# Kernel optimization log

Measured on AMD Instinct MI355X. Metric: run time of the kernel, lower is better.

The kernel has to match this reference:

```python
import jax, jax.numpy as jnp
import numpy as np

BLOCK_SIZE = 32
# E2M1 (FP4) representable magnitudes and rounding midpoints
FP4_GRID = jnp.array([0.0, 0.5, 1.0, 1.5, 2.0, 3.0, 4.0, 6.0], dtype=jnp.float32)
FP4_MIDS = jnp.array([0.25, 0.75, 1.25, 1.75, 2.5, 3.5, 5.0], dtype=jnp.float32)


def quantize_to_mxfp4(w, block_size=BLOCK_SIZE):
    """Quantize (K, N) weight to MXFP4: per-block-of-32 (along K) power-of-2 scale
    + E2M1 codes. Returns dequantized-code tensor q (K//bs, bs, N) and scales
    (K//bs, 1, N) so that dequant = q * scales."""
    K, N = w.shape
    wb = w.reshape(K // block_size, block_size, N)
    amax = jnp.max(jnp.abs(wb), axis=1, keepdims=True)          # (K//bs, 1, N)
    # E8M0 scale: 2^(floor(log2(amax)) - 2) so amax/scale falls in [4, 8) -> clipped to 6
    exp = jnp.floor(jnp.log2(jnp.maximum(amax, 1e-30))) - 2.0
    scales = jnp.exp2(exp)
    x = wb / scales
    idx = jnp.digitize(jnp.abs(x), FP4_MIDS)                    # round-to-nearest FP4 magnitude
    q = jnp.sign(x) * FP4_GRID[idx]
    return q, scales


def mxfp4_matmul(inputs, q, scales, block_size=BLOCK_SIZE):
    """inputs: (..., K); q: (K//bs, bs, N); scales: (K//bs, 1, N)."""
    K = inputs.shape[-1]
    N = q.shape[-1]
    w = (q * scales).reshape(K, N)   # fused dequant (reference form)
    return inputs @ w


def setup_inputs() -> dict:
    key = jax.random.key(0)
    ks = jax.random.split(key, 3)
    B, S, D, F = 4, 2048, 2048, 8192
    inputs = jax.random.normal(ks[0], (B, S, D), dtype=jnp.float32)
    up_kernel = jax.random.normal(ks[1], (D, F), dtype=jnp.float32) * (1.0 / np.sqrt(D))
    down_kernel = jax.random.normal(ks[2], (F, D), dtype=jnp.float32) * (1.0 / np.sqrt(F))
    up_bias = jnp.zeros((F,), dtype=jnp.float32)
    down_bias = jnp.zeros((D,), dtype=jnp.float32)
    return {"inputs": inputs, "up_kernel": up_kernel, "up_bias": up_bias,
            "down_kernel": down_kernel, "down_bias": down_bias}


def reference(inputs, up_kernel, up_bias, down_kernel, down_bias):
    q_up, s_up = quantize_to_mxfp4(up_kernel, BLOCK_SIZE)
    x = mxfp4_matmul(inputs, q_up, s_up, BLOCK_SIZE) + up_bias
    x = jax.nn.gelu(x)
    q_dn, s_dn = quantize_to_mxfp4(down_kernel, BLOCK_SIZE)
    x = mxfp4_matmul(x, q_dn, s_dn, BLOCK_SIZE) + down_bias
    return x
```

## Files before the change

### kernel.cpp

```cpp
#include <hip/hip_runtime.h>
#include <hip/hip_bf16.h>

typedef __bf16 bf16_t;
typedef __attribute__((ext_vector_type(8))) __bf16 bf16x8;
typedef __attribute__((ext_vector_type(4))) float f32x4;
typedef __attribute__((ext_vector_type(4))) unsigned int u32x4;

__device__ __forceinline__ void gload_lds16(const bf16_t* g, bf16_t* l) {
    __builtin_amdgcn_global_load_lds(
        (const __attribute__((address_space(1))) void*)g,
        (__attribute__((address_space(3))) void*)l,
        16, 0, 0);
}

__device__ __forceinline__ float gelu_f(float v) {
    float u = 0.7978845608028654f * (v + 0.044715f * v * v * v);
    float e = __expf(-2.f * u);
    float t = __fdividef(1.f - e, 1.f + e);
    return 0.5f * v * (1.f + t);
}

__global__ void cvt_kernel(const float* __restrict__ in, bf16_t* __restrict__ out, int n) {
    int i = (blockIdx.x * blockDim.x + threadIdx.x) << 3;
    if (i >= n) return;
    const f32x4* p = (const f32x4*)(in + i);
    f32x4 a = __builtin_nontemporal_load(p);
    f32x4 b = __builtin_nontemporal_load(p + 1);
    bf16x8 o;
    o[0] = (bf16_t)a[0]; o[1] = (bf16_t)a[1]; o[2] = (bf16_t)a[2]; o[3] = (bf16_t)a[3];
    o[4] = (bf16_t)b[0]; o[5] = (bf16_t)b[1]; o[6] = (bf16_t)b[2]; o[7] = (bf16_t)b[3];
    *(bf16x8*)(out + i) = o;
}

__global__ void quantize_kernel(const float* __restrict__ w, bf16_t* __restrict__ wt,
                                int K, int N) {
    int tid = blockIdx.x * blockDim.x + threadIdx.x;
    int total = (K >> 5) * N;
    if (tid >= total) return;
    int n = tid % N;
    int b = tid / N;
    const float* src = w + (size_t)b * 32 * N + n;
    float v[32];
    float amax = 0.f;
#pragma unroll
    for (int i = 0; i < 32; ++i) {
        v[i] = __builtin_nontemporal_load(src + (size_t)i * N);
        amax = fmaxf(amax, fabsf(v[i]));
    }
    unsigned eb = (__float_as_uint(amax) >> 23) & 0xFF;
    float scale = __uint_as_float((eb - 2u) << 23);
    float inv   = __uint_as_float((256u - eb) << 23);
    if (amax == 0.f) { scale = 0.f; inv = 0.f; }
    bf16_t dq[32];
#pragma unroll
    for (int i = 0; i < 32; ++i) {
        float x  = v[i] * inv;
        float ax = fabsf(x);
        float q = ax < 0.25f ? 0.0f : ax < 0.75f ? 0.5f : ax < 1.25f ? 1.0f :
                  ax < 1.75f ? 1.5f : ax < 2.5f  ? 2.0f : ax < 3.5f  ? 3.0f :
                  ax < 5.0f  ? 4.0f : 6.0f;
        float d = copysignf(q * scale, x);
        dq[i] = (bf16_t)d;
    }
    bf16_t* dst = wt + (size_t)n * K + b * 32;
#pragma unroll
    for (int j = 0; j < 4; ++j) {
        bf16x8 p;
#pragma unroll
        for (int t = 0; t < 8; ++t) p[t] = dq[j * 8 + t];
        *(bf16x8*)(dst + j * 8) = p;
    }
}

#define VMW4  asm volatile("s_waitcnt vmcnt(4)" ::: "memory")
#define VMW0  asm volatile("s_waitcnt vmcnt(0)" ::: "memory")
#define BARR  asm volatile("s_barrier" ::: "memory")
#define LGKM0 asm volatile("s_waitcnt lgkmcnt(0)" ::: "memory")

#define MFMA_ROW(MI, A0, A1)                                                          \
    acc[MI][0] = __builtin_amdgcn_mfma_f32_16x16x32_bf16(A0, bf00, acc[MI][0],0,0,0); \
    acc[MI][0] = __builtin_amdgcn_mfma_f32_16x16x32_bf16(A1, bf01, acc[MI][0],0,0,0); \
    acc[MI][1] = __builtin_amdgcn_mfma_f32_16x16x32_bf16(A0, bf10, acc[MI][1],0,0,0); \
    acc[MI][1] = __builtin_amdgcn_mfma_f32_16x16x32_bf16(A1, bf11, acc[MI][1],0,0,0); \
    acc[MI][2] = __builtin_amdgcn_mfma_f32_16x16x32_bf16(A0, bf20, acc[MI][2],0,0,0); \
    acc[MI][2] = __builtin_amdgcn_mfma_f32_16x16x32_bf16(A1, bf21, acc[MI][2],0,0,0); \
    acc[MI][3] = __builtin_amdgcn_mfma_f32_16x16x32_bf16(A0, bf30, acc[MI][3],0,0,0); \
    acc[MI][3] = __builtin_amdgcn_mfma_f32_16x16x32_bf16(A1, bf31, acc[MI][3],0,0,0);

#define PHASE(BUF, P, STAGE_STMT, TAIL_STMT)                                          \
  {                                                                                   \
    af00 = lda(BUF, 2*(P),   0); af01 = lda(BUF, 2*(P),   1);                         \
    af10 = lda(BUF, 2*(P)+1, 0); af11 = lda(BUF, 2*(P)+1, 1);                         \
    if ((P) == 0) {                                                                   \
      bf00 = ldb(BUF,0,0); bf01 = ldb(BUF,0,1);                                       \
      bf10 = ldb(BUF,1,0); bf11 = ldb(BUF,1,1);                                       \
      bf20 = ldb(BUF,2,0); bf21 = ldb(BUF,2,1);                                       \
      bf30 = ldb(BUF,3,0); bf31 = ldb(BUF,3,1);                                       \
    }                                                                                 \
    STAGE_STMT;                                                                       \
    BARR;                                                                             \
    LGKM0;                                                                            \
    __builtin_amdgcn_s_setprio(1);                                                    \
    MFMA_ROW(2*(P),   af00, af01);                                                    \
    MFMA_ROW(2*(P)+1, af10, af11);                                                    \
    __builtin_amdgcn_s_setprio(0);                                                    \
    TAIL_STMT;                                                                        \
    BARR;                                                                             \
  }

template <int EPI, int MAP>
__global__ __launch_bounds__(512, 2)
void gemm_kernel(const bf16_t* __restrict__ A, const bf16_t* __restrict__ Bt,
                 const float* __restrict__ bias, void* __restrict__ Cout,
                 int M, int N, int K) {
    __shared__ __align__(16) char smem[131072];
    bf16_t* sAp = (bf16_t*)smem;
    bf16_t* sBp = (bf16_t*)(smem + 65536);
    const int tid     = threadIdx.x;
    const int lane    = tid & 63;
    const int wv      = tid >> 6;
    const int wr      = wv >> 2;
    const int wc      = wv & 3;
    const int laneLow = lane & 15;
    const int laneHi  = lane >> 4;

    int bm, bn;
    const int bid = blockIdx.x;
    if (MAP == 1) {
        const int xcd = bid & 7;
        const int l   = bid >> 3;
        const int r   = l >> 5;
        const int u   = l & 31;
        bm = r * 8 + ((xcd >> 2) << 2) + (u >> 3);
        bn = ((xcd & 3) << 3) + (u & 7);
    } else {
        const int ntn = N >> 8;
        const int nwg = gridDim.x;
        int wg  = (bid & 7) * (nwg >> 3) + (bid >> 3);
        bm = wg / ntn; bn = wg % ntn;
    }

    const int sr8 = lane >> 3;
    const int swz = (((lane & 7) ^ sr8) << 3);
    const bf16_t* aSrc = A  + (size_t)(bm * 256 + wv * 8 + sr8) * K + swz;
    const bf16_t* bSrc = Bt + (size_t)(bn * 256 + wv * 8 + sr8) * K + swz;

    auto stageA = [&](int b, int kt, int h) {
        const bf16_t* s = aSrc + (size_t)(h * 128) * K + kt * 64;
        gload_lds16(s,                &sAp[b * 16384 + (h * 128 + wv * 8) * 64]);
        gload_lds16(s + (size_t)64*K, &sAp[b * 16384 + (h * 128 + 64 + wv * 8) * 64]);
    };
    auto stageB = [&](int b, int kt, int h) {
        const bf16_t* s = bSrc + (size_t)(h * 128) * K + kt * 64;
        gload_lds16(s,                &sBp[b * 16384 + (h * 128 + wv * 8) * 64]);
        gload_lds16(s + (size_t)64*K, &sBp[b * 16384 + (h * 128 + 64 + wv * 8) * 64]);
    };

    const int s7  = laneLow & 7;
    const int xk0 = ((laneHi) ^ s7) << 3;
    const int xk1 = ((4 + laneHi) ^ s7) << 3;
    const int aOffBase = (wr * 128 + laneLow) * 64;
    const int bOffBase = (wc * 64 + laneLow) * 64;
    auto lda = [&](int b, int m, int ks) -> bf16x8 {
        return *(const bf16x8*)(&sAp[b * 16384 + aOffBase + m * 1024 + (ks ? xk1 : xk0)]);
    };
    auto ldb = [&](int b, int n2, int ks) -> bf16x8 {
        return *(const bf16x8*)(&sBp[b * 16384 + bOffBase + n2 * 1024 + (ks ? xk1 : xk0)]);
    };

    f32x4 acc[8][4];
#pragma unroll
    for (int i = 0; i < 8; ++i)
#pragma unroll
        for (int j = 0; j < 4; ++j) acc[i][j] = (f32x4){0.f, 0.f, 0.f, 0.f};

    bf16x8 af00, af01, af10, af11;
    bf16x8 bf00, bf01, bf10, bf11, bf20, bf21, bf30, bf31;

    stageA(0, 0, 0); stageA(0, 0, 1);
    stageB(0, 0, 0); stageB(0, 0, 1);
    stageB(1, 1, 0); stageB(1, 1, 1);
    VMW4;
    BARR;

    const int niter = K >> 7;
    for (int i = 0; i < niter; ++i) {
        const bool nlast = (i + 1 < niter);
        const int kO  = 2 * i + 1;
        const int kN  = 2 * i + 2;
        const int kN1 = 2 * i + 3;
        PHASE(0, 0, stageA(1, kO, 0), ((void)0));
        PHASE(0, 1, stageA(1, kO, 1), ((void)0));
        PHASE(0, 2, if (nlast) stageB(0, kN, 0), ((void)0));
        PHASE(0, 3, if (nlast) stageB(0, kN, 1),
              if (nlast) { VMW4; } else { VMW0; });
        PHASE(1, 0, if (nlast) stageA(0, kN, 0), ((void)0));
        PHASE(1, 1, if (nlast) stageA(0, kN, 1), ((void)0));
        PHASE(1, 2, if (nlast) stageB(1, kN1, 0), ((void)0));
        PHASE(1, 3, if (nlast) stageB(1, kN1, 1),
              if (nlast) { VMW4; });
    }

    if (EPI == 0) {
        bf16_t* sC = (bf16_t*)smem;
#pragma unroll
        for (int n = 0; n < 4; ++n) {
            const int colL = wc * 64 + n * 16 + laneLow;
            const float bv = bias[bn * 256 + colL];
#pragma unroll
            for (int m = 0; m < 8; ++m) {
#pragma unroll
                for (int j = 0; j < 4; ++j) {
                    const int rowL = wr * 128 + m * 16 + (laneHi << 2) + j;
                    float v = acc[m][n][j] + bv;
                    int byte = (rowL << 9) + (colL << 1);
                    byte ^= ((rowL >> 2) & 3) << 5;
                    *(bf16_t*)((char*)sC + byte) = (bf16_t)gelu_f(v);
                }
            }
        }
        LGKM0;
        BARR;
        bf16_t* Cb = (bf16_t*)Cout;
        const size_t rb = (size_t)bm * 256, cb = (size_t)bn * 256;
#pragma unroll
        for (int s = 0; s < 16; ++s) {
            const int row = s * 16 + (tid >> 5);
            int byte = (row << 9) + ((tid & 31) << 4);
            byte ^= ((row >> 2) & 3) << 5;
            u32x4 v = *(const u32x4*)((char*)sC + byte);
            __builtin_nontemporal_store(
                v, (u32x4*)(&Cb[(rb + row) * N + cb + ((tid & 31) << 3)]));
        }
    } else {
        const int r0 = bm * 256 + wr * 128 + (laneHi << 2);
        const int c0 = bn * 256 + wc * 64 + laneLow;
        float* Cf = (float*)Cout;
#pragma unroll
        for (int n = 0; n < 4; ++n) {
            const int col = c0 + n * 16;
            const float bv = bias[col];
#pragma unroll
            for (int m = 0; m < 8; ++m) {
#pragma unroll
                for (int j = 0; j < 4; ++j) {
                    const int row = r0 + m * 16 + j;
                    __builtin_nontemporal_store(acc[m][n][j] + bv,
                                                &Cf[(size_t)row * N + col]);
                }
            }
        }
    }
}

extern "C" void kernel_launch(void* const* d_in, const int* in_sizes, int n_in,
                              void* d_out, int out_size, void* d_ws, size_t ws_size,
                              hipStream_t stream) {
    const float* inputs = (const float*)d_in[0];
    const float* up_w   = (const float*)d_in[1];
    const float* up_b   = (const float*)d_in[2];
    const float* dn_w   = (const float*)d_in[3];
    const float* dn_b   = (const float*)d_in[4];
    float* out = (float*)d_out;

    const int D = in_sizes[4];
    const int F = in_sizes[2];
    const int M = in_sizes[0] / D;

    size_t r0_bytes = (size_t)(M > F ? M : F) * D * 2;
    char* ws = (char*)d_ws;
    bf16_t* in_bf = (bf16_t*)ws;
    bf16_t* wdn_t = (bf16_t*)ws;
    bf16_t* wup_t = (bf16_t*)(ws + r0_bytes);
    bf16_t* mid   = (bf16_t*)(ws + r0_bytes + (size_t)F * D * 2);

    int ncvt = M * D;
    cvt_kernel<<<(ncvt / 8 + 255) / 256, 256, 0, stream>>>(inputs, in_bf, ncvt);
    int qup = (D / 32) * F;
    quantize_kernel<<<(qup + 255) / 256, 256, 0, stream>>>(up_w, wup_t, D, F);
    gemm_kernel<0, 1><<<(M / 256) * (F / 256), 512, 0, stream>>>(
        in_bf, wup_t, up_b, (void*)mid, M, F, D);
    int qdn = (F / 32) * D;
    quantize_kernel<<<(qdn + 255) / 256, 256, 0, stream>>>(dn_w, wdn_t, F, D);
    gemm_kernel<1, 0><<<(M / 256) * (D / 256), 512, 0, stream>>>(
        mid, wdn_t, dn_b, (void*)out, M, D, F);
}
```

Baseline: 548.1 us.

## Pre-tile and swizzle GEMM operands in global memory, merge prep kernels

Inputs, quantized weights and the intermediate activation are now stored in a tiled layout: 256-row by 64-column blocks, contiguous and pre-swizzled. Each GEMM stage load therefore reads one contiguous 16 KB chunk instead of strided rows, and the epilogue writes the intermediate in that same tiled layout. The convert and two quantize kernels are merged into one launch, which requires a separate workspace region for the down weights. The aim is to cut launch overhead and make global loads more coalesced and TLB-friendly, at the cost of more workspace memory.

Result: faster. 536.4 us (-2.1%).

```diff
diff --git a/kernel.cpp b/kernel.cpp
--- a/kernel.cpp
+++ b/kernel.cpp
@@ -20,25 +20,11 @@
     return 0.5f * v * (1.f + t);
 }
 
-__global__ void cvt_kernel(const float* __restrict__ in, bf16_t* __restrict__ out, int n) {
-    int i = (blockIdx.x * blockDim.x + threadIdx.x) << 3;
-    if (i >= n) return;
-    const f32x4* p = (const f32x4*)(in + i);
-    f32x4 a = __builtin_nontemporal_load(p);
-    f32x4 b = __builtin_nontemporal_load(p + 1);
-    bf16x8 o;
-    o[0] = (bf16_t)a[0]; o[1] = (bf16_t)a[1]; o[2] = (bf16_t)a[2]; o[3] = (bf16_t)a[3];
-    o[4] = (bf16_t)b[0]; o[5] = (bf16_t)b[1]; o[6] = (bf16_t)b[2]; o[7] = (bf16_t)b[3];
-    *(bf16x8*)(out + i) = o;
-}
-
-__global__ void quantize_kernel(const float* __restrict__ w, bf16_t* __restrict__ wt,
-                                int K, int N) {
-    int tid = blockIdx.x * blockDim.x + threadIdx.x;
-    int total = (K >> 5) * N;
-    if (tid >= total) return;
-    int n = tid % N;
-    int b = tid / N;
+__device__ __forceinline__ void quant_one(const float* __restrict__ w,
+                                          bf16_t* __restrict__ wt,
+                                          int K, int N, int tix) {
+    int n = tix % N;
+    int b = tix / N;
     const float* src = w + (size_t)b * 32 * N + n;
     float v[32];
     float amax = 0.f;
@@ -62,13 +48,46 @@
         float d = copysignf(q * scale, x);
         dq[i] = (bf16_t)d;
     }
-    bf16_t* dst = wt + (size_t)n * K + b * 32;
+    const int r  = n & 255, rt = n >> 8, kt = b >> 1, ub = (b & 1) * 4;
+    bf16_t* base = wt + (((size_t)rt * (K >> 6) + kt) << 14) + (r << 6);
 #pragma unroll
     for (int j = 0; j < 4; ++j) {
         bf16x8 p;
 #pragma unroll
         for (int t = 0; t < 8; ++t) p[t] = dq[j * 8 + t];
-        *(bf16x8*)(dst + j * 8) = p;
+        *(bf16x8*)(base + (((ub + j) ^ (r & 7)) << 3)) = p;
+    }
+}
+
+__global__ void prep_kernel(const float* __restrict__ in, bf16_t* __restrict__ out,
+                            int ncvt, int cvtB, int dLog,
+                            const float* __restrict__ upw, bf16_t* __restrict__ upwt,
+                            int upK, int upN, int qupB,
+                            const float* __restrict__ dnw, bf16_t* __restrict__ dnwt,
+                            int dnK, int dnN) {
+    int bid = blockIdx.x;
+    if (bid < cvtB) {
+        int i = (bid * blockDim.x + threadIdx.x) << 3;
+        if (i >= ncvt) return;
+        const f32x4* p = (const f32x4*)(in + i);
+        f32x4 a = __builtin_nontemporal_load(p);
+        f32x4 b = __builtin_nontemporal_load(p + 1);
+        bf16x8 o;
+        o[0] = (bf16_t)a[0]; o[1] = (bf16_t)a[1]; o[2] = (bf16_t)a[2]; o[3] = (bf16_t)a[3];
+        o[4] = (bf16_t)b[0]; o[5] = (bf16_t)b[1]; o[6] = (bf16_t)b[2]; o[7] = (bf16_t)b[3];
+        const int row = i >> dLog, d = i & ((1 << dLog) - 1);
+        const int r = row & 255, mt = row >> 8, dt = d >> 6, u = (d >> 3) & 7;
+        size_t off = (((size_t)mt * (1 << (dLog - 6)) + dt) << 14) + (r << 6)
+                     + ((u ^ (r & 7)) << 3);
+        *(bf16x8*)(out + off) = o;
+    } else if (bid < cvtB + qupB) {
+        int tix = (bid - cvtB) * blockDim.x + threadIdx.x;
+        if (tix >= (upK >> 5) * upN) return;
+        quant_one(upw, upwt, upK, upN, tix);
+    } else {
+        int tix = (bid - cvtB - qupB) * blockDim.x + threadIdx.x;
+        if (tix >= (dnK >> 5) * dnN) return;
+        quant_one(dnw, dnwt, dnK, dnN, tix);
     }
 }
 
@@ -140,20 +159,19 @@
         bm = wg / ntn; bn = wg % ntn;
     }
 
-    const int sr8 = lane >> 3;
-    const int swz = (((lane & 7) ^ sr8) << 3);
-    const bf16_t* aSrc = A  + (size_t)(bm * 256 + wv * 8 + sr8) * K + swz;
-    const bf16_t* bSrc = Bt + (size_t)(bn * 256 + wv * 8 + sr8) * K + swz;
+    const int kT = K >> 6;
 
     auto stageA = [&](int b, int kt, int h) {
-        const bf16_t* s = aSrc + (size_t)(h * 128) * K + kt * 64;
-        gload_lds16(s,                &sAp[b * 16384 + (h * 128 + wv * 8) * 64]);
-        gload_lds16(s + (size_t)64*K, &sAp[b * 16384 + (h * 128 + 64 + wv * 8) * 64]);
+        const bf16_t* s = A + (((size_t)bm * kT + kt) << 14)
+                            + ((h * 128 + wv * 8) << 6) + lane * 8;
+        gload_lds16(s,        &sAp[b * 16384 + (h * 128 + wv * 8) * 64]);
+        gload_lds16(s + 4096, &sAp[b * 16384 + (h * 128 + 64 + wv * 8) * 64]);
     };
     auto stageB = [&](int b, int kt, int h) {
-        const bf16_t* s = bSrc + (size_t)(h * 128) * K + kt * 64;
-        gload_lds16(s,                &sBp[b * 16384 + (h * 128 + wv * 8) * 64]);
-        gload_lds16(s + (size_t)64*K, &sBp[b * 16384 + (h * 128 + 64 + wv * 8) * 64]);
+        const bf16_t* s = Bt + (((size_t)bn * kT + kt) << 14)
+                             + ((h * 128 + wv * 8) << 6) + lane * 8;
+        gload_lds16(s,        &sBp[b * 16384 + (h * 128 + wv * 8) * 64]);
+        gload_lds16(s + 4096, &sBp[b * 16384 + (h * 128 + 64 + wv * 8) * 64]);
     };
 
     const int s7  = laneLow & 7;
@@ -183,7 +201,7 @@
     VMW4;
     BARR;
 
-    const int niter = K >> 7;
+    const int niter = kT >> 1;
     for (int i = 0; i < niter; ++i) {
         const bool nlast = (i + 1 < niter);
         const int kO  = 2 * i + 1;
@@ -202,35 +220,35 @@
     }
 
     if (EPI == 0) {
-        bf16_t* sC = (bf16_t*)smem;
+        char* sC = smem;
 #pragma unroll
         for (int n = 0; n < 4; ++n) {
             const int colL = wc * 64 + n * 16 + laneLow;
             const float bv = bias[bn * 256 + colL];
+            const int u6   = (colL >> 3) & 7;
 #pragma unroll
             for (int m = 0; m < 8; ++m) {
 #pragma unroll
                 for (int j = 0; j < 4; ++j) {
                     const int rowL = wr * 128 + m * 16 + (laneHi << 2) + j;
                     float v = acc[m][n][j] + bv;
-                    int byte = (rowL << 9) + (colL << 1);
+                    int byte = ((colL >> 6) << 15) + (rowL << 7)
+                             + ((u6 ^ (rowL & 7)) << 4) + ((colL & 7) << 1);
                     byte ^= ((rowL >> 2) & 3) << 5;
-                    *(bf16_t*)((char*)sC + byte) = (bf16_t)gelu_f(v);
+                    *(bf16_t*)(sC + byte) = (bf16_t)gelu_f(v);
                 }
             }
         }
         LGKM0;
         BARR;
-        bf16_t* Cb = (bf16_t*)Cout;
-        const size_t rb = (size_t)bm * 256, cb = (size_t)bn * 256;
+        char* dst = (char*)Cout + (((size_t)bm * (N >> 6) + bn * 4) << 15);
 #pragma unroll
         for (int s = 0; s < 16; ++s) {
-            const int row = s * 16 + (tid >> 5);
-            int byte = (row << 9) + ((tid & 31) << 4);
-            byte ^= ((row >> 2) & 3) << 5;
-            u32x4 v = *(const u32x4*)((char*)sC + byte);
-            __builtin_nontemporal_store(
-                v, (u32x4*)(&Cb[(rb + row) * N + cb + ((tid & 31) << 3)]));
+            int lin = s * 8192 + tid * 16;
+            int row = (lin >> 7) & 255;
+            int rb  = lin ^ (((row >> 2) & 3) << 5);
+            u32x4 v = *(const u32x4*)(sC + rb);
+            __builtin_nontemporal_store(v, (u32x4*)(dst + lin));
         }
     } else {
         const int r0 = bm * 256 + wr * 128 + (laneHi << 2);
@@ -266,22 +284,28 @@
     const int D = in_sizes[4];
     const int F = in_sizes[2];
     const int M = in_sizes[0] / D;
+    const int dLog = 31 - __builtin_clz((unsigned)D);
 
     size_t r0_bytes = (size_t)(M > F ? M : F) * D * 2;
     char* ws = (char*)d_ws;
     bf16_t* in_bf = (bf16_t*)ws;
-    bf16_t* wdn_t = (bf16_t*)ws;
     bf16_t* wup_t = (bf16_t*)(ws + r0_bytes);
     bf16_t* mid   = (bf16_t*)(ws + r0_bytes + (size_t)F * D * 2);
+    bf16_t* wdn_t = (bf16_t*)(ws + r0_bytes + (size_t)F * D * 2 + (size_t)M * F * 2);
 
     int ncvt = M * D;
-    cvt_kernel<<<(ncvt / 8 + 255) / 256, 256, 0, stream>>>(inputs, in_bf, ncvt);
-    int qup = (D / 32) * F;
-    quantize_kernel<<<(qup + 255) / 256, 256, 0, stream>>>(up_w, wup_t, D, F);
+    int cvtB = ncvt / (8 * 256);
+    int qupB = ((D / 32) * F + 255) / 256;
+    int qdnB = ((F / 32) * D + 255) / 256;
+    prep_kernel<<<cvtB + qupB + qdnB, 256, 0, stream>>>(
+        inputs, in_bf, ncvt, cvtB, dLog,
+        up_w, wup_t, D, F, qupB,
+        dn_w, wdn_t, F, D);
+
     gemm_kernel<0, 1><<<(M / 256) * (F / 256), 512, 0, stream>>>(
         in_bf, wup_t, up_b, (void*)mid, M, F, D);
-    int qdn = (F / 32) * D;
-    quantize_kernel<<<(qdn + 255) / 256, 256, 0, stream>>>(dn_w, wdn_t, F, D);
+
     gemm_kernel<1, 0><<<(M / 256) * (D / 256), 512, 0, stream>>>(
         mid, wdn_t, dn_b, (void*)out, M, D, F);
-}
+    (void)ws_size; (void)n_in; (void)out_size;
+}
```
